# Performance work log

Hardware: AMD Instinct MI355X
Metric: run time of the kernel (lower is better)

The kernel has to match this reference:

```python
import jax, jax.numpy as jnp
import numpy as np

B, S, D, H, E, K = 4, 1024, 1024, 4096, 8, 2


def setup_inputs() -> dict:
    key = jax.random.key(0)
    ks = jax.random.split(key, 10)
    s = 0.02
    return {
        "x": jax.random.normal(ks[0], (B, S, D), jnp.float32),
        "noise": jax.random.normal(ks[1], (B, S, E), jnp.float32),
        "Wg": jax.random.normal(ks[2], (D, E), jnp.float32) * s,
        "bg": jnp.zeros((E,), jnp.float32),
        "Wn": jax.random.normal(ks[3], (D, E), jnp.float32) * s,
        "bn": jnp.zeros((E,), jnp.float32),
        "W1": jax.random.normal(ks[4], (E, D, H), jnp.float32) * s,
        "b1": jnp.zeros((E, H), jnp.float32),
        "W2": jax.random.normal(ks[5], (E, H, D), jnp.float32) * s,
        "b2": jnp.zeros((E, D), jnp.float32),
    }


def reference(x, noise, Wg, bg, Wn, bn, W1, b1, W2, b2):
    # --- noisy top-k gating ---
    logits = x @ Wg + bg                                   # [B,S,E]
    noisy = logits + noise * jax.nn.softplus(x @ Wn + bn)  # [B,S,E]
    topk_vals, topk_idx = jax.lax.top_k(noisy, K)          # [B,S,K]
    weights = jax.nn.softmax(topk_vals, axis=-1)           # [B,S,K]
    oh = jax.nn.one_hot(topk_idx, E, dtype=x.dtype)        # [B,S,K,E]
    mask = oh.sum(axis=-2)                                 # [B,S,E] 0/1 (topk idx distinct)
    w_full = (weights[..., None] * oh).sum(axis=-2)        # [B,S,E] combine weights

    # --- per-expert FFN (dense over experts, selected via w_full) ---
    h = jax.nn.gelu(jnp.einsum('bsd,edh->bseh', x, W1) + b1, approximate=False)
    eout = jnp.einsum('bseh,ehd->bsed', h, W2) + b2        # [B,S,E,D]
    combined = jnp.einsum('bse,bsed->bsd', w_full, eout)   # [B,S,D]

    # --- load balancing loss on clean gate probs ---
    gate_probs = jax.nn.softmax(logits, axis=-1)           # [B,S,E]
    expert_count = mask.sum(axis=(0, 1))                   # [E]
    total_tokens = mask.sum()
    expert_util = expert_count / total_tokens
    load_loss = jnp.sum(expert_util * gate_probs.mean(axis=(0, 1))) * E
    return combined, load_loss
```

## Files before the change

### kernel.cpp

```cpp
#include <hip/hip_runtime.h>
#include <hip/hip_bf16.h>

#define T_TOK 4096
#define D_DIM 1024
#define H_DIM 4096
#define E_EXP 8
#define K_TOP 2
#define TP (T_TOK * K_TOP)
#define BM 128
#define BN 128
#define BKS 32
#define MAX_TILES 72

typedef __attribute__((ext_vector_type(8))) short bf16x8;
typedef __attribute__((ext_vector_type(4))) float f32x4;
typedef __attribute__((ext_vector_type(8))) unsigned short u16x8;
typedef __attribute__((ext_vector_type(4))) unsigned short u16x4;

#define SWZ(row, chunk) ((chunk) ^ (((row) >> 1) & 3))

static __device__ __forceinline__ void gload16(const unsigned short* g, unsigned short* l) {
  __builtin_amdgcn_global_load_lds((const __attribute__((address_space(1))) void*)g,
                                   (__attribute__((address_space(3))) void*)l, 16, 0, 0);
}

static __device__ __forceinline__ unsigned short f2bf(float f) {
  unsigned int bits = __float_as_uint(f);
  unsigned int lsb = (bits >> 16) & 1u;
  bits += 0x7fffu + lsb;
  return (unsigned short)(bits >> 16);
}

static __device__ __forceinline__ float gelu_fast(float u) {
  float z = u * (0.79788456080286536f + 0.0356774081f * u * u);
  float t = __expf(-2.f * z);
  return u / (1.f + t);
}

__global__ __launch_bounds__(256) void convert_x_kernel(
    const float* __restrict__ x, unsigned short* __restrict__ xb) {
  int idx = blockIdx.x * 256 + threadIdx.x;
  float4 v = ((const float4*)x)[idx];
  u16x4 o;
  o[0] = f2bf(v.x); o[1] = f2bf(v.y); o[2] = f2bf(v.z); o[3] = f2bf(v.w);
  *(u16x4*)(xb + (size_t)idx * 4) = o;
}

__global__ __launch_bounds__(256) void transpose_bf16_kernel(
    const float* __restrict__ src, unsigned short* __restrict__ dst, int R, int C) {
  __shared__ float tile[32][129];
  const int e = blockIdx.z;
  const int c0 = blockIdx.x * 32, r0 = blockIdx.y * 128;
  const int tx = threadIdx.x & 31, ty = threadIdx.x >> 5;
  const float* s = src + (size_t)e * R * C;
  unsigned short* d = dst + (size_t)e * R * C;
#pragma unroll
  for (int j = 0; j < 16; ++j) {
    int r = ty + 8 * j;
    tile[tx][r] = s[(size_t)(r0 + r) * C + c0 + tx];
  }
  __syncthreads();
  const int wc = threadIdx.x & 15, cc = threadIdx.x >> 4;
#pragma unroll
  for (int half = 0; half < 2; ++half) {
    int col = cc + 16 * half;
    u16x8 o;
#pragma unroll
    for (int q = 0; q < 8; ++q) o[q] = f2bf(tile[col][wc * 8 + q]);
    *(u16x8*)(&d[(size_t)(c0 + col) * R + r0 + wc * 8]) = o;
  }
}

__global__ __launch_bounds__(256) void gating_kernel(
    const float* __restrict__ x, const float* __restrict__ noise,
    const float* __restrict__ Wg, const float* __restrict__ bg,
    const float* __restrict__ Wn, const float* __restrict__ bn,
    int* __restrict__ tok_e, float* __restrict__ tok_w,
    float* __restrict__ gp_tok, int* __restrict__ counts) {
  const int tid = threadIdx.x, lane = tid & 63, wid = tid >> 6;
  const int t = blockIdx.x * 4 + wid;
  const float* xrow = x + (size_t)t * D_DIM;
  float ag[8] = {0, 0, 0, 0, 0, 0, 0, 0};
  float an[8] = {0, 0, 0, 0, 0, 0, 0, 0};
#pragma unroll 4
  for (int i = 0; i < 16; ++i) {
    int dd = i * 64 + lane;
    float xv = xrow[dd];
    const float4* g4 = (const float4*)(Wg + (size_t)dd * 8);
    const float4* n4 = (const float4*)(Wn + (size_t)dd * 8);
    float4 ga = g4[0], gb = g4[1], na = n4[0], nb = n4[1];
    ag[0] += xv * ga.x; ag[1] += xv * ga.y; ag[2] += xv * ga.z; ag[3] += xv * ga.w;
    ag[4] += xv * gb.x; ag[5] += xv * gb.y; ag[6] += xv * gb.z; ag[7] += xv * gb.w;
    an[0] += xv * na.x; an[1] += xv * na.y; an[2] += xv * na.z; an[3] += xv * na.w;
    an[4] += xv * nb.x; an[5] += xv * nb.y; an[6] += xv * nb.z; an[7] += xv * nb.w;
  }
#pragma unroll
  for (int e = 0; e < 8; ++e) {
    for (int off = 32; off > 0; off >>= 1) {
      ag[e] += __shfl_down(ag[e], off);
      an[e] += __shfl_down(an[e], off);
    }
  }
  if (lane == 0) {
    float logit[8], noisy[8];
#pragma unroll
    for (int e = 0; e < 8; ++e) {
      logit[e] = ag[e] + bg[e];
      float pre = an[e] + bn[e];
      float sp = fmaxf(pre, 0.f) + log1pf(expf(-fabsf(pre)));
      noisy[e] = logit[e] + noise[(size_t)t * 8 + e] * sp;
    }
    float mx = logit[0];
#pragma unroll
    for (int e = 1; e < 8; ++e) mx = fmaxf(mx, logit[e]);
    float s = 0.f, p[8];
#pragma unroll
    for (int e = 0; e < 8; ++e) { p[e] = expf(logit[e] - mx); s += p[e]; }
    float inv = 1.f / s;
#pragma unroll
    for (int e = 0; e < 8; ++e) gp_tok[(size_t)t * 8 + e] = p[e] * inv;
    int i0 = 0; float v0 = noisy[0];
#pragma unroll
    for (int e = 1; e < 8; ++e) if (noisy[e] > v0) { v0 = noisy[e]; i0 = e; }
    int i1 = -1; float v1 = 0.f;
#pragma unroll
    for (int e = 0; e < 8; ++e) {
      if (e == i0) continue;
      if (i1 < 0 || noisy[e] > v1) { v1 = noisy[e]; i1 = e; }
    }
    float e1 = expf(v1 - v0);
    float w0 = 1.f / (1.f + e1);
    float w1 = e1 * w0;
    tok_e[t * 2 + 0] = i0; tok_e[t * 2 + 1] = i1;
    tok_w[t * 2 + 0] = w0; tok_w[t * 2 + 1] = w1;
    atomicAdd(&counts[i0], 1);
    atomicAdd(&counts[i1], 1);
  }
}

__global__ void scan_kernel(const int* __restrict__ counts, int* __restrict__ offsets,
                            int* __restrict__ cursor, int4* __restrict__ tiles,
                            int* __restrict__ ntiles) {
  if (threadIdx.x == 0 && blockIdx.x == 0) {
    int off = 0, nt = 0;
    for (int e = 0; e < E_EXP; ++e) {
      offsets[e] = off;
      int c = counts[e];
      for (int r = 0; r < c; r += BM) {
        tiles[nt] = make_int4(e, off + r, min(BM, c - r), 0);
        ++nt;
      }
      off += c;
      cursor[e] = 0;
    }
    offsets[E_EXP] = off;
    *ntiles = nt;
  }
}

__global__ __launch_bounds__(256) void scatter_kernel(
    const int* __restrict__ tok_e, const float* __restrict__ tok_w,
    const int* __restrict__ offsets, int* __restrict__ cursor,
    int* __restrict__ pair_token, float* __restrict__ pair_w) {
  int t = blockIdx.x * 256 + threadIdx.x;
  if (t >= T_TOK) return;
#pragma unroll
  for (int k = 0; k < 2; ++k) {
    int e = tok_e[t * 2 + k];
    int pos = atomicAdd(&cursor[e], 1);
    int p = offsets[e] + pos;
    pair_token[p] = t;
    pair_w[p] = tok_w[t * 2 + k];
  }
}

__global__ __launch_bounds__(256) void ffn1_kernel(
    const unsigned short* __restrict__ xb,
    const unsigned short* __restrict__ w1t,
    const float* __restrict__ b1,
    const int* __restrict__ pair_token,
    const int4* __restrict__ tiles, const int* __restrict__ ntiles,
    unsigned short* __restrict__ hbuf) {
  const int NB = H_DIM / BN;
  const int nwg = MAX_TILES * NB;
  int bid = blockIdx.x;
  int wg = (bid & 7) * (nwg >> 3) + (bid >> 3);
  int tileId = wg / NB, nb = wg - tileId * NB;
  if (tileId >= *ntiles) return;
  int4 tl = tiles[tileId];
  const int e = tl.x, row0 = tl.y, rows = tl.z;
  const int n0 = nb * BN;

  __shared__ unsigned short As[2][BM * BKS];
  __shared__ unsigned short Bs[2][BN * BKS];

  const int tid = threadIdx.x;
  const int wid = tid >> 6, lane = tid & 63;
  const int sr = tid >> 2;
  const int sc = tid & 3;
  const int scz = SWZ(sr, sc) * 8;

  int r0a = row0 + sr;       if (r0a > TP - 1) r0a = TP - 1;
  int r1a = row0 + sr + 64;  if (r1a > TP - 1) r1a = TP - 1;
  const unsigned short* a0 = xb + (size_t)pair_token[r0a] * D_DIM + scz;
  const unsigned short* a1 = xb + (size_t)pair_token[r1a] * D_DIM + scz;
  const unsigned short* bp0 = w1t + ((size_t)e * H_DIM + (n0 + sr)) * D_DIM + scz;
  const unsigned short* bp1 = w1t + ((size_t)e * H_DIM + (n0 + sr + 64)) * D_DIM + scz;

  const int wbase = wid * 512;
  const int wr = wid >> 1, wc = wid & 1;
  const int lrow = lane & 15, lkc = lane >> 4;

  f32x4 acc[4][4] = {};

  auto stage = [&](int buf, int k0) {
    gload16(a0 + k0, &As[buf][wbase]);
    gload16(a1 + k0, &As[buf][wbase + 2048]);
    gload16(bp0 + k0, &Bs[buf][wbase]);
    gload16(bp1 + k0, &Bs[buf][wbase + 2048]);
  };
  auto compute_step = [&](int buf) {
    bf16x8 af[4], bfr[4];
#pragma unroll
    for (int m = 0; m < 4; ++m) {
      int r = wr * 64 + m * 16 + lrow;
      af[m] = *(const bf16x8*)(&As[buf][r * BKS + SWZ(r, lkc) * 8]);
    }
#pragma unroll
    for (int n = 0; n < 4; ++n) {
      int r = wc * 64 + n * 16 + lrow;
      bfr[n] = *(const bf16x8*)(&Bs[buf][r * BKS + SWZ(r, lkc) * 8]);
    }
#pragma unroll
    for (int m = 0; m < 4; ++m)
#pragma unroll
      for (int n = 0; n < 4; ++n)
        acc[m][n] = __builtin_amdgcn_mfma_f32_16x16x32_bf16(af[m], bfr[n], acc[m][n], 0, 0, 0);
  };

  const int NK = D_DIM / BKS;
  stage(0, 0);
  stage(1, BKS);
  int cur = 0;
  for (int k = 0; k < NK - 1; ++k) {
    asm volatile("s_waitcnt vmcnt(4)" ::: "memory");
    __builtin_amdgcn_s_barrier();
    __builtin_amdgcn_sched_barrier(0);
    compute_step(cur);
    __builtin_amdgcn_sched_barrier(0);
    __builtin_amdgcn_s_barrier();
    if (k < NK - 2) stage(cur, (k + 2) * BKS);
    cur ^= 1;
  }
  asm volatile("s_waitcnt vmcnt(0)" ::: "memory");
  __builtin_amdgcn_s_barrier();
  __builtin_amdgcn_sched_barrier(0);
  compute_step(cur);

  const int colbase = n0 + wc * 64;
#pragma unroll
  for (int n = 0; n < 4; ++n) {
    int colg = colbase + n * 16 + lrow;
    float bias = b1[(size_t)e * H_DIM + colg];
#pragma unroll
    for (int m = 0; m < 4; ++m) {
      int rbase = wr * 64 + m * 16 + (lane >> 4) * 4;
#pragma unroll
      for (int j = 0; j < 4; ++j) {
        int rloc = rbase + j;
        if (rloc < rows) {
          float v = acc[m][n][j] + bias;
          hbuf[(size_t)(row0 + rloc) * H_DIM + colg] = f2bf(gelu_fast(v));
        }
      }
    }
  }
}

__global__ __launch_bounds__(256) void ffn2_kernel(
    const unsigned short* __restrict__ hbuf,
    const unsigned short* __restrict__ w2t,
    const float* __restrict__ b2,
    const int* __restrict__ pair_token, const float* __restrict__ pair_w,
    const int4* __restrict__ tiles, const int* __restrict__ ntiles,
    float* __restrict__ out) {
  const int NB = D_DIM / BN;
  const int nwg = MAX_TILES * NB;
  int bid = blockIdx.x;
  int wg = (bid & 7) * (nwg >> 3) + (bid >> 3);
  int tileId = wg / NB, nb = wg - tileId * NB;
  if (tileId >= *ntiles) return;
  int4 tl = tiles[tileId];
  const int e = tl.x, row0 = tl.y, rows = tl.z;
  const int n0 = nb * BN;

  __shared__ unsigned short As[2][BM * BKS];
  __shared__ unsigned short Bs[2][BN * BKS];
  __shared__ int stok[BM];
  __shared__ float spw[BM];

  const int tid = threadIdx.x;
  if (tid < BM) {
    int rr = row0 + tid; if (rr > TP - 1) rr = TP - 1;
    stok[tid] = pair_token[rr];
    spw[tid] = pair_w[rr];
  }

  const int wid = tid >> 6, lane = tid & 63;
  const int sr = tid >> 2;
  const int sc = tid & 3;
  const int scz = SWZ(sr, sc) * 8;

  int r0a = row0 + sr;       if (r0a > TP - 1) r0a = TP - 1;
  int r1a = row0 + sr + 64;  if (r1a > TP - 1) r1a = TP - 1;
  const unsigned short* a0 = hbuf + (size_t)r0a * H_DIM + scz;
  const unsigned short* a1 = hbuf + (size_t)r1a * H_DIM + scz;
  const unsigned short* bp0 = w2t + ((size_t)e * D_DIM + (n0 + sr)) * H_DIM + scz;
  const unsigned short* bp1 = w2t + ((size_t)e * D_DIM + (n0 + sr + 64)) * H_DIM + scz;

  const int wbase = wid * 512;
  const int wr = wid >> 1, wc = wid & 1;
  const int lrow = lane & 15, lkc = lane >> 4;

  f32x4 acc[4][4] = {};

  auto stage = [&](int buf, int k0) {
    gload16(a0 + k0, &As[buf][wbase]);
    gload16(a1 + k0, &As[buf][wbase + 2048]);
    gload16(bp0 + k0, &Bs[buf][wbase]);
    gload16(bp1 + k0, &Bs[buf][wbase + 2048]);
  };
  auto compute_step = [&](int buf) {
    bf16x8 af[4], bfr[4];
#pragma unroll
    for (int m = 0; m < 4; ++m) {
      int r = wr * 64 + m * 16 + lrow;
      af[m] = *(const bf16x8*)(&As[buf][r * BKS + SWZ(r, lkc) * 8]);
    }
#pragma unroll
    for (int n = 0; n < 4; ++n) {
      int r = wc * 64 + n * 16 + lrow;
      bfr[n] = *(const bf16x8*)(&Bs[buf][r * BKS + SWZ(r, lkc) * 8]);
    }
#pragma unroll
    for (int m = 0; m < 4; ++m)
#pragma unroll
      for (int n = 0; n < 4; ++n)
        acc[m][n] = __builtin_amdgcn_mfma_f32_16x16x32_bf16(af[m], bfr[n], acc[m][n], 0, 0, 0);
  };

  const int NK = H_DIM / BKS;
  stage(0, 0);
  stage(1, BKS);
  int cur = 0;
  for (int k = 0; k < NK - 1; ++k) {
    asm volatile("s_waitcnt vmcnt(4)" ::: "memory");
    __builtin_amdgcn_s_barrier();
    __builtin_amdgcn_sched_barrier(0);
    compute_step(cur);
    __builtin_amdgcn_sched_barrier(0);
    __builtin_amdgcn_s_barrier();
    if (k < NK - 2) stage(cur, (k + 2) * BKS);
    cur ^= 1;
  }
  asm volatile("s_waitcnt vmcnt(0)" ::: "memory");
  __builtin_amdgcn_s_barrier();
  __builtin_amdgcn_sched_barrier(0);
  compute_step(cur);

  const int colbase = n0 + wc * 64;
#pragma unroll
  for (int n = 0; n < 4; ++n) {
    int colg = colbase + n * 16 + lrow;
    float bias = b2[(size_t)e * D_DIM + colg];
#pragma unroll
    for (int m = 0; m < 4; ++m) {
      int rbase = wr * 64 + m * 16 + (lane >> 4) * 4;
#pragma unroll
      for (int j = 0; j < 4; ++j) {
        int rloc = rbase + j;
        if (rloc < rows) {
          float v = acc[m][n][j] + bias;
          unsafeAtomicAdd(&out[(size_t)stok[rloc] * D_DIM + colg], spw[rloc] * v);
        }
      }
    }
  }
}

__global__ __launch_bounds__(256) void loss_kernel(
    const float* __restrict__ gp_tok, const int* __restrict__ counts,
    float* __restrict__ out) {
  __shared__ float red[256];
  const int tid = threadIdx.x;
  float part[8] = {0, 0, 0, 0, 0, 0, 0, 0};
  for (int r = tid; r < T_TOK; r += 256) {
    const float* g = gp_tok + (size_t)r * 8;
#pragma unroll
    for (int e = 0; e < 8; ++e) part[e] += g[e];
  }
  float total[8];
#pragma unroll
  for (int e = 0; e < 8; ++e) {
    red[tid] = part[e];
    __syncthreads();
    for (int s = 128; s > 0; s >>= 1) {
      if (tid < s) red[tid] += red[tid + s];
      __syncthreads();
    }
    if (tid == 0) total[e] = red[0];
    __syncthreads();
  }
  if (tid == 0) {
    float ll = 0.f;
#pragma unroll
    for (int e = 0; e < 8; ++e)
      ll += ((float)counts[e] / (float)TP) * (total[e] / (float)T_TOK);
    out[(size_t)T_TOK * D_DIM] = ll * (float)E_EXP;
  }
}

extern "C" void kernel_launch(void* const* d_in, const int* in_sizes, int n_in,
                              void* d_out, int out_size, void* d_ws, size_t ws_size,
                              hipStream_t stream) {
  (void)in_sizes; (void)n_in; (void)ws_size;
  const float* x     = (const float*)d_in[0];
  const float* noise = (const float*)d_in[1];
  const float* Wg    = (const float*)d_in[2];
  const float* bg    = (const float*)d_in[3];
  const float* Wn    = (const float*)d_in[4];
  const float* bn    = (const float*)d_in[5];
  const float* W1    = (const float*)d_in[6];
  const float* b1    = (const float*)d_in[7];
  const float* W2    = (const float*)d_in[8];
  const float* b2    = (const float*)d_in[9];
  float* out = (float*)d_out;

  char* ws = (char*)d_ws;
  size_t o = 0;
  auto take = [&](size_t b) { size_t r = o; o += (b + 255) & ~(size_t)255; return r; };
  int*   counts     = (int*)(ws + take(16 * 4));
  int*   cursor     = counts + 8;
  int*   offsets    = (int*)(ws + take(9 * 4));
  int*   ntiles     = (int*)(ws + take(4));
  int4*  tiles      = (int4*)(ws + take(MAX_TILES * 16));
  int*   tok_e      = (int*)(ws + take((size_t)TP * 4));
  float* tok_w      = (float*)(ws + take((size_t)TP * 4));
  float* gp_tok     = (float*)(ws + take((size_t)T_TOK * 8 * 4));
  int*   pair_token = (int*)(ws + take((size_t)TP * 4));
  float* pair_w     = (float*)(ws + take((size_t)TP * 4));
  unsigned short* xb  = (unsigned short*)(ws + take((size_t)T_TOK * D_DIM * 2));
  unsigned short* w1t = (unsigned short*)(ws + take((size_t)E_EXP * H_DIM * D_DIM * 2));
  unsigned short* w2t = (unsigned short*)(ws + take((size_t)E_EXP * H_DIM * D_DIM * 2));
  unsigned short* hbuf = (unsigned short*)(ws + take((size_t)TP * H_DIM * 2));

  hipMemsetAsync(d_out, 0, (size_t)out_size * sizeof(float), stream);
  hipMemsetAsync(counts, 0, 16 * 4, stream);

  convert_x_kernel<<<(T_TOK * D_DIM) / (256 * 4), 256, 0, stream>>>(x, xb);
  transpose_bf16_kernel<<<dim3(H_DIM / 32, D_DIM / 128, E_EXP), 256, 0, stream>>>(
      W1, w1t, D_DIM, H_DIM);
  transpose_bf16_kernel<<<dim3(D_DIM / 32, H_DIM / 128, E_EXP), 256, 0, stream>>>(
      W2, w2t, H_DIM, D_DIM);
  gating_kernel<<<T_TOK / 4, 256, 0, stream>>>(x, noise, Wg, bg, Wn, bn,
                                               tok_e, tok_w, gp_tok, counts);
  scan_kernel<<<1, 64, 0, stream>>>(counts, offsets, cursor, tiles, ntiles);
  scatter_kernel<<<T_TOK / 256, 256, 0, stream>>>(tok_e, tok_w, offsets, cursor,
                                                  pair_token, pair_w);
  ffn1_kernel<<<dim3(MAX_TILES * (H_DIM / BN)), 256, 0, stream>>>(
      xb, w1t, b1, pair_token, tiles, ntiles, hbuf);
  ffn2_kernel<<<dim3(MAX_TILES * (D_DIM / BN)), 256, 0, stream>>>(
      hbuf, w2t, b2, pair_token, pair_w, tiles, ntiles, out);
  loss_kernel<<<1, 256, 0, stream>>>(gp_tok, counts, out);
}
```

Measured before the change: 522.7 us.

## Stage FFN1 output through LDS and use 64-row tiles for FFN2

The FFN1 epilogue now writes GELU results into a swizzled LDS tile and then stores them to hbuf as coalesced 16-byte vectors instead of scattered 2-byte stores. FFN2 switches to a separate 64-row tile list and grid, where each wave computes 64x32, doubling the workgroup count for better CU occupancy and load balance. The trade-off is that W2 tiles are re-read twice as often and there is less reuse per MFMA step.

After: 518.8 us. No clear change (-0.8%).

```diff
diff --git a/kernel.cpp b/kernel.cpp
--- a/kernel.cpp
+++ b/kernel.cpp
@@ -9,8 +9,10 @@
 #define TP (T_TOK * K_TOP)
 #define BM 128
 #define BN 128
+#define BM2 64
 #define BKS 32
 #define MAX_TILES 72
+#define MAX_T64 144
 
 typedef __attribute__((ext_vector_type(8))) short bf16x8;
 typedef __attribute__((ext_vector_type(4))) float f32x4;
@@ -140,9 +142,10 @@
 
 __global__ void scan_kernel(const int* __restrict__ counts, int* __restrict__ offsets,
                             int* __restrict__ cursor, int4* __restrict__ tiles,
-                            int* __restrict__ ntiles) {
+                            int* __restrict__ ntiles, int4* __restrict__ tiles64,
+                            int* __restrict__ nt64) {
   if (threadIdx.x == 0 && blockIdx.x == 0) {
-    int off = 0, nt = 0;
+    int off = 0, nt = 0, n64 = 0;
     for (int e = 0; e < E_EXP; ++e) {
       offsets[e] = off;
       int c = counts[e];
@@ -150,11 +153,16 @@
         tiles[nt] = make_int4(e, off + r, min(BM, c - r), 0);
         ++nt;
       }
+      for (int r = 0; r < c; r += BM2) {
+        tiles64[n64] = make_int4(e, off + r, min(BM2, c - r), 0);
+        ++n64;
+      }
       off += c;
       cursor[e] = 0;
     }
     offsets[E_EXP] = off;
     *ntiles = nt;
+    *nt64 = n64;
   }
 }
 
@@ -191,8 +199,9 @@
   const int e = tl.x, row0 = tl.y, rows = tl.z;
   const int n0 = nb * BN;
 
-  __shared__ unsigned short As[2][BM * BKS];
-  __shared__ unsigned short Bs[2][BN * BKS];
+  __shared__ unsigned short sh[16384];
+#define AS1(buf) (sh + (buf) * 4096)
+#define BS1(buf) (sh + 8192 + (buf) * 4096)
 
   const int tid = threadIdx.x;
   const int wid = tid >> 6, lane = tid & 63;
@@ -214,22 +223,22 @@
   f32x4 acc[4][4] = {};
 
   auto stage = [&](int buf, int k0) {
-    gload16(a0 + k0, &As[buf][wbase]);
-    gload16(a1 + k0, &As[buf][wbase + 2048]);
-    gload16(bp0 + k0, &Bs[buf][wbase]);
-    gload16(bp1 + k0, &Bs[buf][wbase + 2048]);
+    gload16(a0 + k0, AS1(buf) + wbase);
+    gload16(a1 + k0, AS1(buf) + wbase + 2048);
+    gload16(bp0 + k0, BS1(buf) + wbase);
+    gload16(bp1 + k0, BS1(buf) + wbase + 2048);
   };
   auto compute_step = [&](int buf) {
     bf16x8 af[4], bfr[4];
 #pragma unroll
     for (int m = 0; m < 4; ++m) {
       int r = wr * 64 + m * 16 + lrow;
-      af[m] = *(const bf16x8*)(&As[buf][r * BKS + SWZ(r, lkc) * 8]);
+      af[m] = *(const bf16x8*)(AS1(buf) + r * BKS + SWZ(r, lkc) * 8);
     }
 #pragma unroll
     for (int n = 0; n < 4; ++n) {
       int r = wc * 64 + n * 16 + lrow;
-      bfr[n] = *(const bf16x8*)(&Bs[buf][r * BKS + SWZ(r, lkc) * 8]);
+      bfr[n] = *(const bf16x8*)(BS1(buf) + r * BKS + SWZ(r, lkc) * 8);
     }
 #pragma unroll
     for (int m = 0; m < 4; ++m)
@@ -257,24 +266,34 @@
   __builtin_amdgcn_sched_barrier(0);
   compute_step(cur);
 
-  const int colbase = n0 + wc * 64;
+  __syncthreads();
 #pragma unroll
   for (int n = 0; n < 4; ++n) {
-    int colg = colbase + n * 16 + lrow;
-    float bias = b1[(size_t)e * H_DIM + colg];
+    int clocal = wc * 64 + n * 16 + lrow;
+    float bias = b1[(size_t)e * H_DIM + n0 + clocal];
+    int chunk = clocal >> 3, within = clocal & 7;
 #pragma unroll
     for (int m = 0; m < 4; ++m) {
-      int rbase = wr * 64 + m * 16 + (lane >> 4) * 4;
 #pragma unroll
       for (int j = 0; j < 4; ++j) {
-        int rloc = rbase + j;
-        if (rloc < rows) {
-          float v = acc[m][n][j] + bias;
-          hbuf[(size_t)(row0 + rloc) * H_DIM + colg] = f2bf(gelu_fast(v));
-        }
+        int rloc = wr * 64 + m * 16 + (lane >> 4) * 4 + j;
+        float v = acc[m][n][j] + bias;
+        sh[rloc * 128 + ((chunk ^ ((rloc >> 1) & 7)) * 8) + within] = f2bf(gelu_fast(v));
       }
     }
   }
+  __syncthreads();
+#pragma unroll
+  for (int it = 0; it < 8; ++it) {
+    int u = tid + 256 * it;
+    int r = u >> 4, cg = u & 15;
+    if (r < rows) {
+      u16x8 v = *(const u16x8*)(&sh[r * 128 + ((cg ^ ((r >> 1) & 7)) * 8)]);
+      *(u16x8*)(&hbuf[(size_t)(row0 + r) * H_DIM + n0 + cg * 8]) = v;
+    }
+  }
+#undef AS1
+#undef BS1
 }
 
 __global__ __launch_bounds__(256) void ffn2_kernel(
@@ -282,70 +301,67 @@
     const unsigned short* __restrict__ w2t,
     const float* __restrict__ b2,
     const int* __restrict__ pair_token, const float* __restrict__ pair_w,
-    const int4* __restrict__ tiles, const int* __restrict__ ntiles,
+    const int4* __restrict__ tiles64, const int* __restrict__ nt64,
     float* __restrict__ out) {
   const int NB = D_DIM / BN;
-  const int nwg = MAX_TILES * NB;
+  const int nwg = MAX_T64 * NB;
   int bid = blockIdx.x;
   int wg = (bid & 7) * (nwg >> 3) + (bid >> 3);
-  int tileId = wg / NB, nb = wg - tileId * NB;
-  if (tileId >= *ntiles) return;
-  int4 tl = tiles[tileId];
+  int tileId = wg >> 3, nb = wg & 7;
+  if (tileId >= *nt64) return;
+  int4 tl = tiles64[tileId];
   const int e = tl.x, row0 = tl.y, rows = tl.z;
   const int n0 = nb * BN;
 
-  __shared__ unsigned short As[2][BM * BKS];
+  __shared__ unsigned short As[2][BM2 * BKS];
   __shared__ unsigned short Bs[2][BN * BKS];
-  __shared__ int stok[BM];
-  __shared__ float spw[BM];
+  __shared__ int stok[BM2];
+  __shared__ float spw[BM2];
 
   const int tid = threadIdx.x;
-  if (tid < BM) {
+  const int wid = tid >> 6, lane = tid & 63;
+  if (tid < BM2) {
     int rr = row0 + tid; if (rr > TP - 1) rr = TP - 1;
     stok[tid] = pair_token[rr];
     spw[tid] = pair_w[rr];
   }
 
-  const int wid = tid >> 6, lane = tid & 63;
-  const int sr = tid >> 2;
-  const int sc = tid & 3;
-  const int scz = SWZ(sr, sc) * 8;
-
-  int r0a = row0 + sr;       if (r0a > TP - 1) r0a = TP - 1;
-  int r1a = row0 + sr + 64;  if (r1a > TP - 1) r1a = TP - 1;
-  const unsigned short* a0 = hbuf + (size_t)r0a * H_DIM + scz;
-  const unsigned short* a1 = hbuf + (size_t)r1a * H_DIM + scz;
-  const unsigned short* bp0 = w2t + ((size_t)e * D_DIM + (n0 + sr)) * H_DIM + scz;
-  const unsigned short* bp1 = w2t + ((size_t)e * D_DIM + (n0 + sr + 64)) * H_DIM + scz;
-
-  const int wbase = wid * 512;
-  const int wr = wid >> 1, wc = wid & 1;
+  const int sc = lane & 3;
+  const int sra = wid * 16 + (lane >> 2);
+  const int srb0 = wid * 32 + (lane >> 2);
+  const int srb1 = srb0 + 16;
+  int pa = row0 + sra; if (pa > TP - 1) pa = TP - 1;
+  const unsigned short* ap  = hbuf + (size_t)pa * H_DIM + SWZ(sra, sc) * 8;
+  const unsigned short* bp0 = w2t + ((size_t)e * D_DIM + (n0 + srb0)) * H_DIM + SWZ(srb0, sc) * 8;
+  const unsigned short* bp1 = w2t + ((size_t)e * D_DIM + (n0 + srb1)) * H_DIM + SWZ(srb1, sc) * 8;
+  const int abase = wid * 512;
+  const int bbase = wid * 1024;
+
   const int lrow = lane & 15, lkc = lane >> 4;
 
-  f32x4 acc[4][4] = {};
+  f32x4 acc[4][2] = {};
 
   auto stage = [&](int buf, int k0) {
-    gload16(a0 + k0, &As[buf][wbase]);
-    gload16(a1 + k0, &As[buf][wbase + 2048]);
-    gload16(bp0 + k0, &Bs[buf][wbase]);
-    gload16(bp1 + k0, &Bs[buf][wbase + 2048]);
+    gload16(ap + k0, &As[buf][abase]);
+    gload16(bp0 + k0, &Bs[buf][bbase]);
+    gload16(bp1 + k0, &Bs[buf][bbase + 512]);
   };
   auto compute_step = [&](int buf) {
-    bf16x8 af[4], bfr[4];
+    bf16x8 af[4], bfr[2];
 #pragma unroll
     for (int m = 0; m < 4; ++m) {
-      int r = wr * 64 + m * 16 + lrow;
+      int r = m * 16 + lrow;
       af[m] = *(const bf16x8*)(&As[buf][r * BKS + SWZ(r, lkc) * 8]);
     }
 #pragma unroll
-    for (int n = 0; n < 4; ++n) {
-      int r = wc * 64 + n * 16 + lrow;
+    for (int n = 0; n < 2; ++n) {
+      int r = wid * 32 + n * 16 + lrow;
       bfr[n] = *(const bf16x8*)(&Bs[buf][r * BKS + SWZ(r, lkc) * 8]);
     }
 #pragma unroll
     for (int m = 0; m < 4; ++m)
 #pragma unroll
-      for (int n = 0; n < 4; ++n)
+      for (int n = 0; n < 2; ++n)
         acc[m][n] = __builtin_amdgcn_mfma_f32_16x16x32_bf16(af[m], bfr[n], acc[m][n], 0, 0, 0);
   };
 
@@ -354,7 +370,7 @@
   stage(1, BKS);
   int cur = 0;
   for (int k = 0; k < NK - 1; ++k) {
-    asm volatile("s_waitcnt vmcnt(4)" ::: "memory");
+    asm volatile("s_waitcnt vmcnt(3)" ::: "memory");
     __builtin_amdgcn_s_barrier();
     __builtin_amdgcn_sched_barrier(0);
     compute_step(cur);
@@ -368,14 +384,13 @@
   __builtin_amdgcn_sched_barrier(0);
   compute_step(cur);
 
-  const int colbase = n0 + wc * 64;
-#pragma unroll
-  for (int n = 0; n < 4; ++n) {
-    int colg = colbase + n * 16 + lrow;
+#pragma unroll
+  for (int n = 0; n < 2; ++n) {
+    int colg = n0 + wid * 32 + n * 16 + lrow;
     float bias = b2[(size_t)e * D_DIM + colg];
 #pragma unroll
     for (int m = 0; m < 4; ++m) {
-      int rbase = wr * 64 + m * 16 + (lane >> 4) * 4;
+      int rbase = m * 16 + (lane >> 4) * 4;
 #pragma unroll
       for (int j = 0; j < 4; ++j) {
         int rloc = rbase + j;
@@ -443,7 +458,9 @@
   int*   cursor     = counts + 8;
   int*   offsets    = (int*)(ws + take(9 * 4));
   int*   ntiles     = (int*)(ws + take(4));
+  int*   nt64       = (int*)(ws + take(4));
   int4*  tiles      = (int4*)(ws + take(MAX_TILES * 16));
+  int4*  tiles64    = (int4*)(ws + take(MAX_T64 * 16));
   int*   tok_e      = (int*)(ws + take((size_t)TP * 4));
   float* tok_w      = (float*)(ws + take((size_t)TP * 4));
   float* gp_tok     = (float*)(ws + take((size_t)T_TOK * 8 * 4));
@@ -464,12 +481,13 @@
       W2, w2t, H_DIM, D_DIM);
   gating_kernel<<<T_TOK / 4, 256, 0, stream>>>(x, noise, Wg, bg, Wn, bn,
                                                tok_e, tok_w, gp_tok, counts);
-  scan_kernel<<<1, 64, 0, stream>>>(counts, offsets, cursor, tiles, ntiles);
+  scan_kernel<<<1, 64, 0, stream>>>(counts, offsets, cursor, tiles, ntiles,
+                                    tiles64, nt64);
   scatter_kernel<<<T_TOK / 256, 256, 0, stream>>>(tok_e, tok_w, offsets, cursor,
                                                   pair_token, pair_w);
   ffn1_kernel<<<dim3(MAX_TILES * (H_DIM / BN)), 256, 0, stream>>>(
       xb, w1t, b1, pair_token, tiles, ntiles, hbuf);
-  ffn2_kernel<<<dim3(MAX_TILES * (D_DIM / BN)), 256, 0, stream>>>(
-      hbuf, w2t, b2, pair_token, pair_w, tiles, ntiles, out);
+  ffn2_kernel<<<dim3(MAX_T64 * (D_DIM / BN)), 256, 0, stream>>>(
+      hbuf, w2t, b2, pair_token, pair_w, tiles64, nt64, out);
   loss_kernel<<<1, 256, 0, stream>>>(gp_tok, counts, out);
 }
```

## Widen FFN1 tile to 256 columns and stage GELU output through LDS

Applied to the files above, without the earlier changes.

The FFN1 grouped GEMM tile grows from 128x128 to 128x256, so each wave computes a 64x128 sub-tile with 32 accumulators. Each A fragment now feeds twice as many MFMAs and half as many workgroups are launched, which raises arithmetic intensity and reuse of the gathered x rows. The epilogue writes bias+GELU bf16 results into a swizzled LDS buffer and then stores them to hbuf as 16-byte vectors instead of scattered 2-byte stores. The cost is much higher register pressure, which may lower occupancy, plus more LDS and extra barriers in the epilogue.

Measured after the change: 601.3 us. 1.15x slower.

```diff
diff --git a/kernel.cpp b/kernel.cpp
--- a/kernel.cpp
+++ b/kernel.cpp
@@ -9,6 +9,7 @@
 #define TP (T_TOK * K_TOP)
 #define BM 128
 #define BN 128
+#define BN1 256
 #define BKS 32
 #define MAX_TILES 72
 
@@ -181,7 +182,7 @@
     const int* __restrict__ pair_token,
     const int4* __restrict__ tiles, const int* __restrict__ ntiles,
     unsigned short* __restrict__ hbuf) {
-  const int NB = H_DIM / BN;
+  const int NB = H_DIM / BN1;
   const int nwg = MAX_TILES * NB;
   int bid = blockIdx.x;
   int wg = (bid & 7) * (nwg >> 3) + (bid >> 3);
@@ -189,10 +190,11 @@
   if (tileId >= *ntiles) return;
   int4 tl = tiles[tileId];
   const int e = tl.x, row0 = tl.y, rows = tl.z;
-  const int n0 = nb * BN;
-
-  __shared__ unsigned short As[2][BM * BKS];
-  __shared__ unsigned short Bs[2][BN * BKS];
+  const int n0 = nb * BN1;
+
+  __shared__ unsigned short sh[24576];
+#define AS1(buf) (sh + (buf) * 4096)
+#define BS1(buf) (sh + 8192 + (buf) * 8192)
 
   const int tid = threadIdx.x;
   const int wid = tid >> 6, lane = tid & 63;
@@ -204,38 +206,39 @@
   int r1a = row0 + sr + 64;  if (r1a > TP - 1) r1a = TP - 1;
   const unsigned short* a0 = xb + (size_t)pair_token[r0a] * D_DIM + scz;
   const unsigned short* a1 = xb + (size_t)pair_token[r1a] * D_DIM + scz;
-  const unsigned short* bp0 = w1t + ((size_t)e * H_DIM + (n0 + sr)) * D_DIM + scz;
-  const unsigned short* bp1 = w1t + ((size_t)e * H_DIM + (n0 + sr + 64)) * D_DIM + scz;
+  const unsigned short* bq[4];
+#pragma unroll
+  for (int q = 0; q < 4; ++q)
+    bq[q] = w1t + ((size_t)e * H_DIM + (n0 + sr + 64 * q)) * D_DIM + scz;
 
   const int wbase = wid * 512;
   const int wr = wid >> 1, wc = wid & 1;
   const int lrow = lane & 15, lkc = lane >> 4;
 
-  f32x4 acc[4][4] = {};
+  f32x4 acc[4][8] = {};
 
   auto stage = [&](int buf, int k0) {
-    gload16(a0 + k0, &As[buf][wbase]);
-    gload16(a1 + k0, &As[buf][wbase + 2048]);
-    gload16(bp0 + k0, &Bs[buf][wbase]);
-    gload16(bp1 + k0, &Bs[buf][wbase + 2048]);
+    gload16(a0 + k0, AS1(buf) + wbase);
+    gload16(a1 + k0, AS1(buf) + wbase + 2048);
+#pragma unroll
+    for (int q = 0; q < 4; ++q)
+      gload16(bq[q] + k0, BS1(buf) + wbase + q * 2048);
   };
   auto compute_step = [&](int buf) {
-    bf16x8 af[4], bfr[4];
+    bf16x8 af[4];
 #pragma unroll
     for (int m = 0; m < 4; ++m) {
       int r = wr * 64 + m * 16 + lrow;
-      af[m] = *(const bf16x8*)(&As[buf][r * BKS + SWZ(r, lkc) * 8]);
-    }
-#pragma unroll
-    for (int n = 0; n < 4; ++n) {
-      int r = wc * 64 + n * 16 + lrow;
-      bfr[n] = *(const bf16x8*)(&Bs[buf][r * BKS + SWZ(r, lkc) * 8]);
-    }
-#pragma unroll
-    for (int m = 0; m < 4; ++m)
-#pragma unroll
-      for (int n = 0; n < 4; ++n)
-        acc[m][n] = __builtin_amdgcn_mfma_f32_16x16x32_bf16(af[m], bfr[n], acc[m][n], 0, 0, 0);
+      af[m] = *(const bf16x8*)(AS1(buf) + r * BKS + SWZ(r, lkc) * 8);
+    }
+#pragma unroll
+    for (int n = 0; n < 8; ++n) {
+      int r = wc * 128 + n * 16 + lrow;
+      bf16x8 bf = *(const bf16x8*)(BS1(buf) + r * BKS + SWZ(r, lkc) * 8);
+#pragma unroll
+      for (int m = 0; m < 4; ++m)
+        acc[m][n] = __builtin_amdgcn_mfma_f32_16x16x32_bf16(af[m], bf, acc[m][n], 0, 0, 0);
+    }
   };
 
   const int NK = D_DIM / BKS;
@@ -243,7 +246,7 @@
   stage(1, BKS);
   int cur = 0;
   for (int k = 0; k < NK - 1; ++k) {
-    asm volatile("s_waitcnt vmcnt(4)" ::: "memory");
+    asm volatile("s_waitcnt vmcnt(6)" ::: "memory");
     __builtin_amdgcn_s_barrier();
     __builtin_amdgcn_sched_barrier(0);
     compute_step(cur);
@@ -257,24 +260,40 @@
   __builtin_amdgcn_sched_barrier(0);
   compute_step(cur);
 
-  const int colbase = n0 + wc * 64;
-#pragma unroll
-  for (int n = 0; n < 4; ++n) {
-    int colg = colbase + n * 16 + lrow;
-    float bias = b1[(size_t)e * H_DIM + colg];
-#pragma unroll
-    for (int m = 0; m < 4; ++m) {
-      int rbase = wr * 64 + m * 16 + (lane >> 4) * 4;
-#pragma unroll
-      for (int j = 0; j < 4; ++j) {
-        int rloc = rbase + j;
-        if (rloc < rows) {
-          float v = acc[m][n][j] + bias;
-          hbuf[(size_t)(row0 + rloc) * H_DIM + colg] = f2bf(gelu_fast(v));
+  __syncthreads();
+#pragma unroll
+  for (int h = 0; h < 2; ++h) {
+    if (wc == h) {
+#pragma unroll
+      for (int n = 0; n < 8; ++n) {
+        int cl = n * 16 + lrow;
+        float bias = b1[(size_t)e * H_DIM + n0 + h * 128 + cl];
+        int chunk = cl >> 3, within = cl & 7;
+#pragma unroll
+        for (int m = 0; m < 4; ++m) {
+#pragma unroll
+          for (int j = 0; j < 4; ++j) {
+            int rloc = wr * 64 + m * 16 + (lane >> 4) * 4 + j;
+            float v = acc[m][n][j] + bias;
+            sh[rloc * 128 + ((chunk ^ ((rloc >> 1) & 7)) * 8) + within] = f2bf(gelu_fast(v));
+          }
         }
       }
     }
-  }
+    __syncthreads();
+#pragma unroll
+    for (int it = 0; it < 8; ++it) {
+      int u = tid + 256 * it;
+      int r = u >> 4, cg = u & 15;
+      if (r < rows) {
+        u16x8 v = *(const u16x8*)(&sh[r * 128 + ((cg ^ ((r >> 1) & 7)) * 8)]);
+        *(u16x8*)(&hbuf[(size_t)(row0 + r) * H_DIM + n0 + h * 128 + cg * 8]) = v;
+      }
+    }
+    __syncthreads();
+  }
+#undef AS1
+#undef BS1
 }
 
 __global__ __launch_bounds__(256) void ffn2_kernel(
@@ -467,7 +486,7 @@
   scan_kernel<<<1, 64, 0, stream>>>(counts, offsets, cursor, tiles, ntiles);
   scatter_kernel<<<T_TOK / 256, 256, 0, stream>>>(tok_e, tok_w, offsets, cursor,
                                                   pair_token, pair_w);
-  ffn1_kernel<<<dim3(MAX_TILES * (H_DIM / BN)), 256, 0, stream>>>(
+  ffn1_kernel<<<dim3(MAX_TILES * (H_DIM / BN1)), 256, 0, stream>>>(
       xb, w1t, b1, pair_token, tiles, ntiles, hbuf);
   ffn2_kernel<<<dim3(MAX_TILES * (D_DIM / BN)), 256, 0, stream>>>(
       hbuf, w2t, b2, pair_token, pair_w, tiles, ntiles, out);
```
